# Performance work log

Measured on AMD Instinct MI355X. Metric: run time of the kernel, lower is better.

The kernel has to match this reference:

```python
import jax, jax.numpy as jnp
import numpy as np
from math import sqrt

NUM_HEADS = 16
NUM_KV_HEADS = 4
ROPE_BASE = 10000.0


def setup_inputs() -> dict:
    key = jax.random.key(0)
    ks = jax.random.split(key, 9)
    B, S, E = 4, 2048, 2048
    KV_DIM = NUM_KV_HEADS * (E // NUM_HEADS)  # 512
    s = 0.02
    return {
        "x": jax.random.normal(ks[0], (B, S, E), jnp.float32),
        "wq": jax.random.normal(ks[1], (E, E), jnp.float32) * s,
        "bq": jnp.zeros((E,), jnp.float32),
        "wk": jax.random.normal(ks[2], (KV_DIM, E), jnp.float32) * s,
        "bk": jnp.zeros((KV_DIM,), jnp.float32),
        "wv": jax.random.normal(ks[3], (KV_DIM, E), jnp.float32) * s,
        "bv": jnp.zeros((KV_DIM,), jnp.float32),
        "wo": jax.random.normal(ks[4], (E, E), jnp.float32) * s,
        "bo": jnp.zeros((E,), jnp.float32),
    }


def _rope_cos_sin(seq_len, head_dim, dtype):
    inv_freq = 1.0 / (ROPE_BASE ** (jnp.arange(0, head_dim, 2, dtype=jnp.float32) / head_dim))
    pos = jnp.arange(seq_len, dtype=jnp.float32)
    freqs = pos[:, None] * inv_freq[None, :]            # [S, D/2]
    emb = jnp.concatenate([freqs, freqs], axis=-1)      # [S, D]
    return jnp.cos(emb).astype(dtype), jnp.sin(emb).astype(dtype)


def _apply_rope(t, cos, sin):
    # t: [B, H, S, D]; cos/sin: [S, D]
    d2 = t.shape[-1] // 2
    rot = jnp.concatenate([-t[..., d2:], t[..., :d2]], axis=-1)
    return t * cos[None, None, :, :] + rot * sin[None, None, :, :]


def reference(x, wq, bq, wk, bk, wv, bv, wo, bo):
    B, S, E = x.shape
    H, KV = NUM_HEADS, NUM_KV_HEADS
    D = E // H
    G = H // KV

    q = (x @ wq.T + bq).reshape(B, S, H, D).transpose(0, 2, 1, 3)   # [B,H,S,D]
    k = (x @ wk.T + bk).reshape(B, S, KV, D).transpose(0, 2, 1, 3)  # [B,KV,S,D]
    v = (x @ wv.T + bv).reshape(B, S, KV, D).transpose(0, 2, 1, 3)

    cos, sin = _rope_cos_sin(S, D, x.dtype)
    q = _apply_rope(q, cos, sin)
    k = _apply_rope(k, cos, sin)

    # GQA: expand each kv head group_size times (contiguous repeat)
    k = jnp.repeat(k, G, axis=1)  # [B,H,S,D]
    v = jnp.repeat(v, G, axis=1)

    scores = jnp.einsum("bhqd,bhkd->bhqk", q, k)
    causal = jnp.triu(jnp.ones((S, S), dtype=bool), k=1)
    scores = jnp.where(causal[None, None, :, :], -jnp.inf, scores)
    attn = jax.nn.softmax(scores / sqrt(D), axis=-1)
    out = jnp.einsum("bhqk,bhkd->bhqd", attn, v)        # [B,H,S,D]
    out = out.transpose(0, 2, 1, 3).reshape(B, S, E)
    return out @ wo.T + bo
```

## Files before the change

kernel.cpp:

```cpp
#include <hip/hip_runtime.h>
#include <stdint.h>
#include <math.h>

typedef __attribute__((ext_vector_type(8))) short s16x8;
typedef __attribute__((ext_vector_type(4))) short s16x4;
typedef __attribute__((ext_vector_type(4))) float f32x4;
typedef __attribute__((ext_vector_type(16))) float f32x16;

#define NEGH (-1.0e30f)

__device__ __forceinline__ short f2bf(float f) {
  union { float f; unsigned int i; } c; c.f = f;
  unsigned int lsb = (c.i >> 16) & 1u;
  c.i += 0x7fffu + lsb;
  return (short)(c.i >> 16);
}
__device__ __forceinline__ float bf2f(short u) {
  union { unsigned int i; float f; } c;
  c.i = ((unsigned int)(unsigned short)u) << 16;
  return c.f;
}

#define GLOAD_LDS16(gp, lp)                                                  \
  __builtin_amdgcn_global_load_lds(                                          \
      (__attribute__((address_space(1))) void*)(void*)(gp),                  \
      (__attribute__((address_space(3))) void*)(lp), 16, 0, 0)

__global__ __launch_bounds__(256) void cvt_kernel(const float* __restrict__ in,
                                                  short* __restrict__ out)
{
  const size_t i = ((size_t)blockIdx.x * 256 + threadIdx.x) * 4;
  const float4 v = *(const float4*)(in + i);
  s16x4 o = { f2bf(v.x), f2bf(v.y), f2bf(v.z), f2bf(v.w) };
  *(s16x4*)(out + i) = o;
}

__global__ __launch_bounds__(256) void wcvt_kernel(
    const float* __restrict__ wq, const float* __restrict__ wk,
    const float* __restrict__ wv, short* __restrict__ wqb,
    short* __restrict__ wkb, short* __restrict__ wvb,
    float2* __restrict__ tab)
{
  const int bid = blockIdx.x;
  if (bid < 6144) {
    const float* in; short* out; int lb;
    if (bid < 4096)      { in = wq; out = wqb; lb = bid; }
    else if (bid < 5120) { in = wk; out = wkb; lb = bid - 4096; }
    else                 { in = wv; out = wvb; lb = bid - 5120; }
    const size_t i = ((size_t)lb * 256 + threadIdx.x) * 4;
    const float4 v = *(const float4*)(in + i);
    s16x4 o = { f2bf(v.x), f2bf(v.y), f2bf(v.z), f2bf(v.w) };
    *(s16x4*)(out + i) = o;
  } else {
    const int i = (bid - 6144) * 256 + threadIdx.x;
    const int d = i & 63;
    const float fr = (float)(i >> 6) * exp2f((float)d * -0.20762050593048584f);
    float sn, cs;
    sincosf(fr, &sn, &cs);
    tab[i] = make_float2(cs, sn);
  }
}

__global__ __launch_bounds__(256) void gemm_bt(
    const short* __restrict__ A, const short* __restrict__ W,
    const float* __restrict__ bias, const float* __restrict__ bias2,
    void* __restrict__ C, void* __restrict__ C2,
    int M, int N, int K, int omode)
{
  __shared__ __align__(16) short As[128 * 64];
  __shared__ __align__(16) short Bs[128 * 64];

  const int t = threadIdx.x;
  const int l = t & 63;
  const int w = t >> 6;
  const int lane16 = l & 15;
  const int quad = l >> 4;
  const int wm = w >> 1, wn = w & 1;

  int bx = blockIdx.x, by = blockIdx.y;
  if (gridDim.x == 8 && gridDim.y == 64) {
    const int lid = blockIdx.x + 8 * blockIdx.y;
    const int xcd = lid & 7, idx = lid >> 3;
    by = xcd * 8 + (idx >> 3);
    bx = idx & 7;
  }
  const int mb0 = by * 128;
  const int nb0 = bx * 128;

  const f32x4 zero = {0.f, 0.f, 0.f, 0.f};
  f32x4 acc[4][4];
#pragma unroll
  for (int i = 0; i < 4; ++i)
#pragma unroll
    for (int j = 0; j < 4; ++j) acc[i][j] = zero;

  const int sr = t >> 3;
  const int sp = t & 7;
  const short* Ag = A + (size_t)(mb0 + sr) * K + sp * 8;
  const short* Wg = W + (size_t)(nb0 + sr) * K + sp * 8;
  short* Al = As + t * 8;
  short* Bl = Bs + t * 8;

  const int nkt = K >> 6;
  for (int kt = 0; kt < nkt; ++kt) {
    __syncthreads();
    const int kof = kt * 64;
#pragma unroll
    for (int it = 0; it < 4; ++it) {
      GLOAD_LDS16(Ag + kof + (size_t)(it * 32) * K, Al + it * 2048);
      GLOAD_LDS16(Wg + kof + (size_t)(it * 32) * K, Bl + it * 2048);
    }
    __syncthreads();
#pragma unroll
    for (int kk = 0; kk < 2; ++kk) {
      s16x8 af[4], bf[4];
#pragma unroll
      for (int mi = 0; mi < 4; ++mi)
        af[mi] = *(const s16x8*)&As[(wm * 64 + mi * 16 + lane16) * 64 +
                                    kk * 32 + quad * 8];
#pragma unroll
      for (int ni = 0; ni < 4; ++ni)
        bf[ni] = *(const s16x8*)&Bs[(wn * 64 + ni * 16 + lane16) * 64 +
                                    kk * 32 + quad * 8];
#pragma unroll
      for (int mi = 0; mi < 4; ++mi)
#pragma unroll
        for (int ni = 0; ni < 4; ++ni)
          acc[mi][ni] = __builtin_amdgcn_mfma_f32_16x16x32_bf16(
              af[mi], bf[ni], acc[mi][ni], 0, 0, 0);
    }
  }

#pragma unroll
  for (int ni = 0; ni < 4; ++ni) {
    const int n = nb0 + wn * 64 + ni * 16 + lane16;
    const float bvx = (omode == 3 && n >= 512) ? bias2[n - 512] : bias[n];
#pragma unroll
    for (int mi = 0; mi < 4; ++mi) {
      const int m0 = mb0 + wm * 64 + mi * 16 + quad * 4;
#pragma unroll
      for (int r = 0; r < 4; ++r) {
        const int m = m0 + r;
        const float v = acc[mi][ni][r] + bvx;
        if (omode == 0) {
          ((short*)C)[(size_t)m * N + n] = f2bf(v);
        } else if (omode == 1) {
          ((float*)C)[(size_t)m * N + n] = v;
        } else {
          if (n < 512) ((short*)C)[(size_t)m * 512 + n] = f2bf(v);
          else         ((short*)C2)[(size_t)m * 512 + (n - 512)] = f2bf(v);
        }
      }
    }
  }
}

__global__ __launch_bounds__(512, 2) void gemm256_bt(
    const short* __restrict__ A, const short* __restrict__ W,
    const float* __restrict__ bias, void* __restrict__ C,
    int M, int N, int K, int omode)
{
  __shared__ __align__(16) short Asm[2 * 16384];
  __shared__ __align__(16) short Bsm[2 * 16384];

  const int t = threadIdx.x;
  const int l = t & 63;
  const int w = t >> 6;
  const int lane16 = l & 15;
  const int quad = l >> 4;
  const int wm = w >> 2;
  const int wn = w & 3;

  int bx = blockIdx.x, by = blockIdx.y;
  if (gridDim.x == 8 && gridDim.y == 32) {
    const int bid = blockIdx.y * 8 + blockIdx.x;
    const int xcd = bid & 7, idx = bid >> 3;
    const int xc = xcd & 3, yc = xcd >> 2;
    bx = xc * 2 + (idx & 1);
    by = yc * 16 + (idx >> 1);
  }
  const int mb0 = by * 256;
  const int nb0 = bx * 256;

  const f32x4 zero = {0.f, 0.f, 0.f, 0.f};
  f32x4 acc[8][4];
#pragma unroll
  for (int i = 0; i < 8; ++i)
#pragma unroll
    for (int j = 0; j < 4; ++j) acc[i][j] = zero;

  const int srow = t >> 2;
  const int scs = (t & 3) ^ ((t >> 3) & 3);
  const short* Ag = A + (size_t)(mb0 + srow) * K + scs * 8;
  const short* Wg = W + (size_t)(nb0 + srow) * K + scs * 8;
  const size_t rstep = (size_t)128 * K;

#define STAGE_A(b, kt, kh)                                                    \
  do {                                                                        \
    const size_t ko_ = (size_t)(kt) * 64 + (kh) * 32;                         \
    GLOAD_LDS16(Ag + ko_,         Asm + (b) * 16384 + (kh) * 8192 + t * 8);   \
    GLOAD_LDS16(Ag + ko_ + rstep, Asm + (b) * 16384 + (kh) * 8192 + 4096 + t * 8); \
  } while (0)
#define STAGE_B(b, kt, kh)                                                    \
  do {                                                                        \
    const size_t ko_ = (size_t)(kt) * 64 + (kh) * 32;                         \
    GLOAD_LDS16(Wg + ko_,         Bsm + (b) * 16384 + (kh) * 8192 + t * 8);   \
    GLOAD_LDS16(Wg + ko_ + rstep, Bsm + (b) * 16384 + (kh) * 8192 + 4096 + t * 8); \
  } while (0)

#define VMW6                                                                  \
  asm volatile("s_waitcnt vmcnt(6)" ::: "memory");                            \
  __builtin_amdgcn_sched_barrier(0);

  s16x8 bfr[4];

#define DO_PHASE(BUF, KK, MG, READB, STAGE_STMT, VM_STMT)                     \
  {                                                                           \
    const short* Abase = Asm + (BUF) * 16384 + (KK) * 8192;                   \
    const short* Bbase = Bsm + (BUF) * 16384 + (KK) * 8192;                   \
    if (READB) {                                                              \
      _Pragma("unroll")                                                       \
      for (int ni = 0; ni < 4; ++ni) {                                        \
        const int nr = wn * 64 + ni * 16 + lane16;                            \
        bfr[ni] = *(const s16x8*)(Bbase + nr * 32 +                           \
                                  ((quad ^ ((nr >> 1) & 3)) << 3));           \
      }                                                                       \
    }                                                                         \
    s16x8 afr[4];                                                             \
    _Pragma("unroll")                                                         \
    for (int mi2 = 0; mi2 < 4; ++mi2) {                                       \
      const int mr = wm * 128 + (MG) * 64 + mi2 * 16 + lane16;                \
      afr[mi2] = *(const s16x8*)(Abase + mr * 32 +                            \
                                 ((quad ^ ((mr >> 1) & 3)) << 3));            \
    }                                                                         \
    STAGE_STMT;                                                               \
    __builtin_amdgcn_s_barrier();                                             \
    asm volatile("s_waitcnt lgkmcnt(0)" ::: "memory");                        \
    __builtin_amdgcn_sched_barrier(0);                                        \
    __builtin_amdgcn_s_setprio(1);                                            \
    _Pragma("unroll")                                                         \
    for (int mi2 = 0; mi2 < 4; ++mi2)                                         \
      _Pragma("unroll")                                                       \
      for (int ni = 0; ni < 4; ++ni)                                          \
        acc[(MG) * 4 + mi2][ni] = __builtin_amdgcn_mfma_f32_16x16x32_bf16(    \
            afr[mi2], bfr[ni], acc[(MG) * 4 + mi2][ni], 0, 0, 0);             \
    __builtin_amdgcn_s_setprio(0);                                            \
    VM_STMT                                                                   \
    __builtin_amdgcn_s_barrier();                                             \
  }

  const int NT = K >> 6;

  STAGE_B(0, 0, 0); STAGE_A(0, 0, 0); STAGE_B(0, 0, 1); STAGE_A(0, 0, 1);
  STAGE_B(1, 1, 0); STAGE_A(1, 1, 0); STAGE_B(1, 1, 1);
  asm volatile("s_waitcnt vmcnt(6)" ::: "memory");
  __builtin_amdgcn_sched_barrier(0);
  __builtin_amdgcn_s_barrier();

  for (int i2 = 0; i2 < NT; i2 += 2) {
    const int tp1 = (i2 + 1 < NT) ? i2 + 1 : NT - 1;
    const int tp2 = (i2 + 2 < NT) ? i2 + 2 : NT - 1;
    const int tp3 = (i2 + 3 < NT) ? i2 + 3 : NT - 1;
    DO_PHASE(0, 0, 0, true,  STAGE_A(1, tp1, 1), )
    DO_PHASE(0, 0, 1, false, STAGE_B(0, tp2, 0), )
    DO_PHASE(0, 1, 0, true,  STAGE_A(0, tp2, 0), )
    DO_PHASE(0, 1, 1, false, STAGE_B(0, tp2, 1), VMW6)
    DO_PHASE(1, 0, 0, true,  STAGE_A(0, tp2, 1), )
    DO_PHASE(1, 0, 1, false, STAGE_B(1, tp3, 0), )
    DO_PHASE(1, 1, 0, true,  STAGE_A(1, tp3, 0), )
    DO_PHASE(1, 1, 1, false, STAGE_B(1, tp3, 1), VMW6)
  }

#pragma unroll
  for (int ni = 0; ni < 4; ++ni) {
    const int n = nb0 + wn * 64 + ni * 16 + lane16;
    const float bv = bias[n];
#pragma unroll
    for (int mi = 0; mi < 8; ++mi) {
      const int m0 = mb0 + wm * 128 + mi * 16 + quad * 4;
#pragma unroll
      for (int r = 0; r < 4; ++r) {
        const float v = acc[mi][ni][r] + bv;
        if (omode == 0) ((short*)C)[(size_t)(m0 + r) * N + n] = f2bf(v);
        else            ((float*)C)[(size_t)(m0 + r) * N + n] = v;
      }
    }
  }
#undef DO_PHASE
#undef STAGE_A
#undef STAGE_B
#undef VMW6
}

__global__ __launch_bounds__(256) void rope_kernel(short* __restrict__ buf,
                                                   int lognh,
                                                   const float2* __restrict__ tab)
{
  const int idx = blockIdx.x * 256 + threadIdx.x;
  const int d = idx & 63;
  const int rest = idx >> 6;
  const int row = rest >> lognh;
  const int pos = row & 2047;
  const float2 cssn = tab[(pos << 6) | d];
  const float cs = cssn.x, sn = cssn.y;
  const size_t base = (size_t)rest * 128 + d;
  const float lo = bf2f(buf[base]);
  const float hi = bf2f(buf[base + 64]);
  buf[base]      = f2bf(lo * cs - hi * sn);
  buf[base + 64] = f2bf(hi * cs + lo * sn);
}

__global__ __launch_bounds__(256) void trans_kernel(const short* __restrict__ in,
                                                    short* __restrict__ out)
{
  __shared__ short T[64 * 72];
  const int t = threadIdx.x;
  const int ms = blockIdx.x * 64;
  const int ns = blockIdx.y * 64;
  const int b = ms >> 11;
  const int sl = ms & 2047;
  const int r = t >> 3, sg = t & 7;
#pragma unroll
  for (int j = 0; j < 2; ++j) {
    const uint4 v = *(const uint4*)(in + (size_t)(ms + r + 32 * j) * 512 + ns + sg * 8);
    *(uint4*)&T[(r + 32 * j) * 72 + sg * 8] = v;
  }
  __syncthreads();
#pragma unroll
  for (int j = 0; j < 2; ++j) {
    const int nr = r + 32 * j;
    s16x8 v;
#pragma unroll
    for (int i = 0; i < 8; ++i) v[i] = T[(sg * 8 + i) * 72 + nr];
    *(s16x8*)(out + ((size_t)(b * 512 + ns + nr)) * 2048 + sl + sg * 8) = v;
  }
}

__global__ __launch_bounds__(256, 2) void attn_kernel(
    const short* __restrict__ qg, const short* __restrict__ kg,
    const short* __restrict__ vtg, short* __restrict__ og,
    const float2* __restrict__ tab)
{
  __shared__ __align__(16) short Ksm[2 * 64 * 128];
  __shared__ __align__(16) short Vsm[2 * 128 * 64];

  const int t = threadIdx.x;
  const int l = t & 63;
  const int w = t >> 6;
  const int l31 = l & 31;
  const int h2 = l >> 5;

  const int lid = blockIdx.x + 8 * (blockIdx.y + 16 * blockIdx.z);
  const int xcd = lid & 7, idx = lid >> 3;
  const int g = xcd * 2 + (idx >> 5);
  const int wv_ = idx & 31;
  const int b = g >> 2, kv = g & 3;
  const int h = kv * 4 + (wv_ >> 3);
  const int jb = wv_ & 7;

  const int krow0 = t >> 4, kseg = (t & 15) ^ (t >> 4);
  const int vrow0 = t >> 3, vseg = (t & 7) ^ ((t >> 3) & 7);

  const short* kbaseptr = kg + ((size_t)(b * 2048)) * 512 + kv * 128;
  const short* vbaseptr = vtg + ((size_t)(b * 512 + kv * 128)) * 2048;

  const float SC = 0.08838834764831845f * 1.4426950408889634f;
  const f32x16 zero16 = {0.f,0.f,0.f,0.f,0.f,0.f,0.f,0.f,
                         0.f,0.f,0.f,0.f,0.f,0.f,0.f,0.f};

#define STAGET(c)                                                             \
  do {                                                                        \
    GLOAD_LDS16(ksrc,          Ksm + (c) * 8192 + t * 8);                     \
    GLOAD_LDS16(ksrc + 8192,   Ksm + (c) * 8192 + 2048 + t * 8);              \
    GLOAD_LDS16(ksrc + 16384,  Ksm + (c) * 8192 + 4096 + t * 8);              \
    GLOAD_LDS16(ksrc + 24576,  Ksm + (c) * 8192 + 6144 + t * 8);              \
    GLOAD_LDS16(vsrc,          Vsm + (c) * 8192 + t * 8);                     \
    GLOAD_LDS16(vsrc + 65536,  Vsm + (c) * 8192 + 2048 + t * 8);              \
    GLOAD_LDS16(vsrc + 131072, Vsm + (c) * 8192 + 4096 + t * 8);              \
    GLOAD_LDS16(vsrc + 196608, Vsm + (c) * 8192 + 6144 + t * 8);              \
    ksrc += 64 * 512;                                                         \
    vsrc += 64;                                                               \
  } while (0)

  for (int sp2 = 0; sp2 < 2; ++sp2) {
    const int jj = sp2 ? (15 - jb) : jb;
    const int qb0 = jj * 128;
    const int qw0 = qb0 + w * 32;
    const int qmaxw = qw0 + 31;
    const int ntl = 2 * jj + 2;

    const short* ksrc = kbaseptr + (size_t)krow0 * 512 + kseg * 8;
    const short* vsrc = vbaseptr + (size_t)vrow0 * 2048 + vseg * 8;

    s16x8 qf[8];
    {
      const int pos = qw0 + l31;
      const short* qrow =
          qg + ((size_t)(b * 2048 + pos)) * 2048 + h * 128 + 8 * h2;
      s16x8 qr[8];
#pragma unroll
      for (int m = 0; m < 8; ++m) qr[m] = *(const s16x8*)(qrow + 16 * m);
      const float2* tb = tab + (((size_t)pos) << 6) + 8 * h2;
#pragma unroll
      for (int m = 0; m < 4; ++m) {
        float lo[8], hi[8];
#pragma unroll
        for (int j = 0; j < 8; ++j) {
          const float2 cs2 = tb[16 * m + j];
          const float l0 = bf2f(qr[m][j]);
          const float h0 = bf2f(qr[m + 4][j]);
          lo[j] = l0 * cs2.x - h0 * cs2.y;
          hi[j] = h0 * cs2.x + l0 * cs2.y;
        }
        union { unsigned int u[4]; s16x8 v; } plo, phi;
#pragma unroll
        for (int j = 0; j < 4; ++j) {
          asm("v_cvt_pk_bf16_f32 %0, %1, %2"
              : "=v"(plo.u[j]) : "v"(lo[2 * j]), "v"(lo[2 * j + 1]));
          asm("v_cvt_pk_bf16_f32 %0, %1, %2"
              : "=v"(phi.u[j]) : "v"(hi[2 * j]), "v"(hi[2 * j + 1]));
        }
        qf[m] = plo.v;
        qf[m + 4] = phi.v;
      }
    }

    f32x16 o32[4];
#pragma unroll
    for (int nb = 0; nb < 4; ++nb) o32[nb] = zero16;
    float m_i = NEGH, l_i = 0.f;

    STAGET(0);
    __syncthreads();
    int cur = 0;

    for (int tl = 0; tl < ntl; ++tl) {
      const int kbase = tl * 64;
      if (tl + 1 < ntl) STAGET(cur ^ 1);

      if (kbase <= qmaxw) {
        const short* Kb = Ksm + cur * 8192;
        const short* Vb = Vsm + cur * 8192;

        f32x16 st0 = zero16, st1 = zero16;
        __builtin_amdgcn_s_setprio(1);
#pragma unroll
        for (int m = 0; m < 8; ++m) {
          const int ch = ((2 * m + h2) ^ (l & 15)) * 8;
          const s16x8 a0 = *(const s16x8*)&Kb[l31 * 128 + ch];
          const s16x8 a1 = *(const s16x8*)&Kb[(32 + l31) * 128 + ch];
          st0 = __builtin_amdgcn_mfma_f32_32x32x16_bf16(a0, qf[m], st0, 0, 0, 0);
          st1 = __builtin_amdgcn_mfma_f32_32x32x16_bf16(a1, qf[m], st1, 0, 0, 0);
        }
        __builtin_amdgcn_s_setprio(0);

        const bool maskt = (kbase + 63 > qw0);
        const int qabs = qw0 + l31;
        if (maskt) {
#pragma unroll
          for (int r = 0; r < 16; ++r) {
            const int krow = (r & 3) + 8 * (r >> 2) + 4 * h2;
            if (kbase + krow > qabs) st0[r] = NEGH;
            if (kbase + 32 + krow > qabs) st1[r] = NEGH;
          }
        }
        float tm = NEGH;
#pragma unroll
        for (int r = 0; r < 16; ++r) tm = fmaxf(tm, fmaxf(st0[r], st1[r]));
        float tl_ = fmaxf(tm, __shfl_xor(tm, 32));
        const float mnew = fmaxf(m_i, tl_);
        if (!__all(tl_ <= m_i)) {
          const float alpha = exp2f((m_i - mnew) * SC);
          l_i *= alpha;
#pragma unroll
          for (int r = 0; r < 16; ++r) {
            const int qrow = (r & 3) + 8 * (r >> 2) + 4 * h2;
            const float ar = __shfl(alpha, qrow);
#pragma unroll
            for (int nb = 0; nb < 4; ++nb) o32[nb][r] *= ar;
          }
        }
        m_i = mnew;
        const float mS = mnew * SC;
        float rs = 0.f;
#pragma unroll
        for (int r = 0; r < 16; ++r) {
          st0[r] = exp2f(fmaf(st0[r], SC, -mS));
          st1[r] = exp2f(fmaf(st1[r], SC, -mS));
          rs += st0[r] + st1[r];
        }
        rs += __shfl_xor(rs, 32);
        l_i += rs;

        unsigned int wA[8], wB[8];
#pragma unroll
        for (int a = 0; a < 4; ++a) {
          asm("v_cvt_pk_bf16_f32 %0, %1, %2"
              : "=v"(wA[a]) : "v"(st0[4 * a]), "v"(st0[4 * a + 1]));
          asm("v_cvt_pk_bf16_f32 %0, %1, %2"
              : "=v"(wB[a]) : "v"(st0[4 * a + 2]), "v"(st0[4 * a + 3]));
          asm("v_cvt_pk_bf16_f32 %0, %1, %2"
              : "=v"(wA[a + 4]) : "v"(st1[4 * a]), "v"(st1[4 * a + 1]));
          asm("v_cvt_pk_bf16_f32 %0, %1, %2"
              : "=v"(wB[a + 4]) : "v"(st1[4 * a + 2]), "v"(st1[4 * a + 3]));
        }

        __builtin_amdgcn_s_setprio(1);
#pragma unroll
        for (int kk = 0; kk < 4; ++kk) {
          const int i0 = 2 * (kk & 1) + 4 * (kk >> 1);
          const unsigned int sA = h2 ? wA[i0] : wA[i0 + 1];
          const unsigned int sB = h2 ? wB[i0] : wB[i0 + 1];
          const unsigned int rA = (unsigned int)__shfl_xor((int)sA, 32);
          const unsigned int rB = (unsigned int)__shfl_xor((int)sB, 32);
          union { unsigned int u[4]; s16x8 v; } pfu;
          pfu.u[0] = h2 ? rA : wA[i0];
          pfu.u[1] = h2 ? rB : wB[i0];
          pfu.u[2] = h2 ? wA[i0 + 1] : rA;
          pfu.u[3] = h2 ? wB[i0 + 1] : rB;
          const s16x8 pf = pfu.v;
#pragma unroll
          for (int nb = 0; nb < 4; ++nb) {
            const s16x8 vf = *(const s16x8*)&Vb[(nb * 32 + l31) * 64 +
                                                (((2 * kk + h2) ^ (l & 7)) * 8)];
            o32[nb] = __builtin_amdgcn_mfma_f32_32x32x16_bf16(pf, vf, o32[nb],
                                                              0, 0, 0);
          }
        }
        __builtin_amdgcn_s_setprio(0);
      }

      __syncthreads();
      cur ^= 1;
    }

#pragma unroll
    for (int r = 0; r < 16; ++r) {
      const int qrow = (r & 3) + 8 * (r >> 2) + 4 * h2;
      const float lr = __shfl(l_i, qrow);
      const float inv = 1.f / lr;
      const size_t base =
          ((size_t)(b * 2048 + qw0 + qrow)) * 2048 + h * 128 + l31;
#pragma unroll
      for (int nb = 0; nb < 4; ++nb)
        og[base + nb * 32] = f2bf(o32[nb][r] * inv);
    }
  }
#undef STAGET
}

extern "C" void kernel_launch(void* const* d_in, const int* in_sizes, int n_in,
                              void* d_out, int out_size, void* d_ws,
                              size_t ws_size, hipStream_t stream)
{
  const float* x  = (const float*)d_in[0];
  const float* wq = (const float*)d_in[1];
  const float* bq = (const float*)d_in[2];
  const float* wk = (const float*)d_in[3];
  const float* bk = (const float*)d_in[4];
  const float* wv = (const float*)d_in[5];
  const float* bv = (const float*)d_in[6];
  const float* wo = (const float*)d_in[7];
  const float* bo = (const float*)d_in[8];
  float* out = (float*)d_out;

  char* ws = (char*)d_ws;
  short* xb  = (short*)ws;
  short* wqb = (short*)(ws + (32ull << 20));
  short* wkb = (short*)(ws + (40ull << 20));
  short* wvb = (short*)(ws + (42ull << 20));
  short* qws = (short*)(ws + (44ull << 20));
  float2* tab = (float2*)(ws + (76ull << 20));
  short* wob = xb;
  short* kws = (short*)d_out;
  short* vtw = (short*)((char*)d_out + (8ull << 20));
  short* vtmp = (short*)((char*)d_out + (16ull << 20));

  const dim3 blk(256);
  cvt_kernel<<<16384, blk, 0, stream>>>(x, xb);
  wcvt_kernel<<<6656, blk, 0, stream>>>(wq, wk, wv, wqb, wkb, wvb, tab);
  gemm256_bt<<<dim3(8, 32), dim3(512), 0, stream>>>(xb, wqb, bq, qws, 8192, 2048, 2048, 0);
  gemm_bt<<<dim3(8, 64), blk, 0, stream>>>(xb, wkb, bk, bv, kws, vtmp, 8192, 1024, 2048, 3);
  trans_kernel<<<dim3(128, 8), blk, 0, stream>>>(vtmp, vtw);
  rope_kernel<<<8192, blk, 0, stream>>>(kws, 2, tab);
  cvt_kernel<<<4096, blk, 0, stream>>>(wo, wob);
  attn_kernel<<<dim3(8, 16, 4), blk, 0, stream>>>(qws, kws, vtw, qws, tab);
  gemm256_bt<<<dim3(8, 32), dim3(512), 0, stream>>>(qws, wob, bo, out, 8192, 2048, 2048, 1);
}
```

Before: 495.1 us.

## Single-buffer attention K/V tiles with split K/V staging, one query block per CTA

```diff
diff --git a/kernel.cpp b/kernel.cpp
--- a/kernel.cpp
+++ b/kernel.cpp
@@ -341,8 +341,8 @@
     const short* __restrict__ vtg, short* __restrict__ og,
     const float2* __restrict__ tab)
 {
-  __shared__ __align__(16) short Ksm[2 * 64 * 128];
-  __shared__ __align__(16) short Vsm[2 * 128 * 64];
+  __shared__ __align__(16) short Ksm[64 * 128];
+  __shared__ __align__(16) short Vsm[128 * 64];
 
   const int t = threadIdx.x;
   const int l = t & 63;
@@ -350,13 +350,13 @@
   const int l31 = l & 31;
   const int h2 = l >> 5;
 
-  const int lid = blockIdx.x + 8 * (blockIdx.y + 16 * blockIdx.z);
+  const int lid = blockIdx.x + 16 * (blockIdx.y + 16 * blockIdx.z);
   const int xcd = lid & 7, idx = lid >> 3;
-  const int g = xcd * 2 + (idx >> 5);
-  const int wv_ = idx & 31;
+  const int g = xcd * 2 + (idx >> 6);
+  const int wv_ = idx & 63;
   const int b = g >> 2, kv = g & 3;
-  const int h = kv * 4 + (wv_ >> 3);
-  const int jb = wv_ & 7;
+  const int h = kv * 4 + (wv_ >> 4);
+  const int jj = wv_ & 15;
 
   const int krow0 = t >> 4, kseg = (t & 15) ^ (t >> 4);
   const int vrow0 = t >> 3, vseg = (t & 7) ^ ((t >> 3) & 7);
@@ -368,185 +368,188 @@
   const f32x16 zero16 = {0.f,0.f,0.f,0.f,0.f,0.f,0.f,0.f,
                          0.f,0.f,0.f,0.f,0.f,0.f,0.f,0.f};
 
-#define STAGET(c)                                                             \
+#define STAGE_K()                                                             \
   do {                                                                        \
-    GLOAD_LDS16(ksrc,          Ksm + (c) * 8192 + t * 8);                     \
-    GLOAD_LDS16(ksrc + 8192,   Ksm + (c) * 8192 + 2048 + t * 8);              \
-    GLOAD_LDS16(ksrc + 16384,  Ksm + (c) * 8192 + 4096 + t * 8);              \
-    GLOAD_LDS16(ksrc + 24576,  Ksm + (c) * 8192 + 6144 + t * 8);              \
-    GLOAD_LDS16(vsrc,          Vsm + (c) * 8192 + t * 8);                     \
-    GLOAD_LDS16(vsrc + 65536,  Vsm + (c) * 8192 + 2048 + t * 8);              \
-    GLOAD_LDS16(vsrc + 131072, Vsm + (c) * 8192 + 4096 + t * 8);              \
-    GLOAD_LDS16(vsrc + 196608, Vsm + (c) * 8192 + 6144 + t * 8);              \
+    GLOAD_LDS16(ksrc,          Ksm + t * 8);                                  \
+    GLOAD_LDS16(ksrc + 8192,   Ksm + 2048 + t * 8);                           \
+    GLOAD_LDS16(ksrc + 16384,  Ksm + 4096 + t * 8);                           \
+    GLOAD_LDS16(ksrc + 24576,  Ksm + 6144 + t * 8);                           \
     ksrc += 64 * 512;                                                         \
+  } while (0)
+#define STAGE_V()                                                             \
+  do {                                                                        \
+    GLOAD_LDS16(vsrc,          Vsm + t * 8);                                  \
+    GLOAD_LDS16(vsrc + 65536,  Vsm + 2048 + t * 8);                           \
+    GLOAD_LDS16(vsrc + 131072, Vsm + 4096 + t * 8);                           \
+    GLOAD_LDS16(vsrc + 196608, Vsm + 6144 + t * 8);                           \
     vsrc += 64;                                                               \
   } while (0)
 
-  for (int sp2 = 0; sp2 < 2; ++sp2) {
-    const int jj = sp2 ? (15 - jb) : jb;
-    const int qb0 = jj * 128;
-    const int qw0 = qb0 + w * 32;
-    const int qmaxw = qw0 + 31;
-    const int ntl = 2 * jj + 2;
-
-    const short* ksrc = kbaseptr + (size_t)krow0 * 512 + kseg * 8;
-    const short* vsrc = vbaseptr + (size_t)vrow0 * 2048 + vseg * 8;
-
-    s16x8 qf[8];
-    {
-      const int pos = qw0 + l31;
-      const short* qrow =
-          qg + ((size_t)(b * 2048 + pos)) * 2048 + h * 128 + 8 * h2;
-      s16x8 qr[8];
-#pragma unroll
-      for (int m = 0; m < 8; ++m) qr[m] = *(const s16x8*)(qrow + 16 * m);
-      const float2* tb = tab + (((size_t)pos) << 6) + 8 * h2;
-#pragma unroll
-      for (int m = 0; m < 4; ++m) {
-        float lo[8], hi[8];
-#pragma unroll
-        for (int j = 0; j < 8; ++j) {
-          const float2 cs2 = tb[16 * m + j];
-          const float l0 = bf2f(qr[m][j]);
-          const float h0 = bf2f(qr[m + 4][j]);
-          lo[j] = l0 * cs2.x - h0 * cs2.y;
-          hi[j] = h0 * cs2.x + l0 * cs2.y;
+  const int qb0 = jj * 128;
+  const int qw0 = qb0 + w * 32;
+  const int qmaxw = qw0 + 31;
+  const int ntl = 2 * jj + 2;
+
+  const short* ksrc = kbaseptr + (size_t)krow0 * 512 + kseg * 8;
+  const short* vsrc = vbaseptr + (size_t)vrow0 * 2048 + vseg * 8;
+
+  s16x8 qf[8];
+  {
+    const int pos = qw0 + l31;
+    const short* qrow =
+        qg + ((size_t)(b * 2048 + pos)) * 2048 + h * 128 + 8 * h2;
+    s16x8 qr[8];
+#pragma unroll
+    for (int m = 0; m < 8; ++m) qr[m] = *(const s16x8*)(qrow + 16 * m);
+    const float2* tb = tab + (((size_t)pos) << 6) + 8 * h2;
+#pragma unroll
+    for (int m = 0; m < 4; ++m) {
+      float lo[8], hi[8];
+#pragma unroll
+      for (int j = 0; j < 8; ++j) {
+        const float2 cs2 = tb[16 * m + j];
+        const float l0 = bf2f(qr[m][j]);
+        const float h0 = bf2f(qr[m + 4][j]);
+        lo[j] = l0 * cs2.x - h0 * cs2.y;
+        hi[j] = h0 * cs2.x + l0 * cs2.y;
+      }
+      union { unsigned int u[4]; s16x8 v; } plo, phi;
+#pragma unroll
+      for (int j = 0; j < 4; ++j) {
+        asm("v_cvt_pk_bf16_f32 %0, %1, %2"
+            : "=v"(plo.u[j]) : "v"(lo[2 * j]), "v"(lo[2 * j + 1]));
+        asm("v_cvt_pk_bf16_f32 %0, %1, %2"
+            : "=v"(phi.u[j]) : "v"(hi[2 * j]), "v"(hi[2 * j + 1]));
+      }
+      qf[m] = plo.v;
+      qf[m + 4] = phi.v;
+    }
+  }
+
+  f32x16 o32[4];
+#pragma unroll
+  for (int nb = 0; nb < 4; ++nb) o32[nb] = zero16;
+  float m_i = NEGH, l_i = 0.f;
+
+  STAGE_K();
+  STAGE_V();
+  __syncthreads();
+
+  for (int tl = 0; tl < ntl; ++tl) {
+    const int kbase = tl * 64;
+    const bool cmp = (kbase <= qmaxw);
+
+    f32x16 st0 = zero16, st1 = zero16;
+    if (cmp) {
+      __builtin_amdgcn_s_setprio(1);
+#pragma unroll
+      for (int m = 0; m < 8; ++m) {
+        const int ch = ((2 * m + h2) ^ (l & 15)) * 8;
+        const s16x8 a0 = *(const s16x8*)&Ksm[l31 * 128 + ch];
+        const s16x8 a1 = *(const s16x8*)&Ksm[(32 + l31) * 128 + ch];
+        st0 = __builtin_amdgcn_mfma_f32_32x32x16_bf16(a0, qf[m], st0, 0, 0, 0);
+        st1 = __builtin_amdgcn_mfma_f32_32x32x16_bf16(a1, qf[m], st1, 0, 0, 0);
+      }
+      __builtin_amdgcn_s_setprio(0);
+    }
+
+    __syncthreads();
+    if (tl + 1 < ntl) STAGE_K();
+
+    if (cmp) {
+      const bool maskt = (kbase + 63 > qw0);
+      const int qabs = qw0 + l31;
+      if (maskt) {
+#pragma unroll
+        for (int r = 0; r < 16; ++r) {
+          const int krow = (r & 3) + 8 * (r >> 2) + 4 * h2;
+          if (kbase + krow > qabs) st0[r] = NEGH;
+          if (kbase + 32 + krow > qabs) st1[r] = NEGH;
         }
-        union { unsigned int u[4]; s16x8 v; } plo, phi;
-#pragma unroll
-        for (int j = 0; j < 4; ++j) {
-          asm("v_cvt_pk_bf16_f32 %0, %1, %2"
-              : "=v"(plo.u[j]) : "v"(lo[2 * j]), "v"(lo[2 * j + 1]));
-          asm("v_cvt_pk_bf16_f32 %0, %1, %2"
-              : "=v"(phi.u[j]) : "v"(hi[2 * j]), "v"(hi[2 * j + 1]));
+      }
+      float tm = NEGH;
+#pragma unroll
+      for (int r = 0; r < 16; ++r) tm = fmaxf(tm, fmaxf(st0[r], st1[r]));
+      float tl_ = fmaxf(tm, __shfl_xor(tm, 32));
+      const float mnew = fmaxf(m_i, tl_);
+      if (!__all(tl_ <= m_i)) {
+        const float alpha = exp2f((m_i - mnew) * SC);
+        l_i *= alpha;
+#pragma unroll
+        for (int r = 0; r < 16; ++r) {
+          const int qrow = (r & 3) + 8 * (r >> 2) + 4 * h2;
+          const float ar = __shfl(alpha, qrow);
+#pragma unroll
+          for (int nb = 0; nb < 4; ++nb) o32[nb][r] *= ar;
         }
-        qf[m] = plo.v;
-        qf[m + 4] = phi.v;
-      }
-    }
-
-    f32x16 o32[4];
-#pragma unroll
-    for (int nb = 0; nb < 4; ++nb) o32[nb] = zero16;
-    float m_i = NEGH, l_i = 0.f;
-
-    STAGET(0);
+      }
+      m_i = mnew;
+      const float mS = mnew * SC;
+      float rs = 0.f;
+#pragma unroll
+      for (int r = 0; r < 16; ++r) {
+        st0[r] = exp2f(fmaf(st0[r], SC, -mS));
+        st1[r] = exp2f(fmaf(st1[r], SC, -mS));
+        rs += st0[r] + st1[r];
+      }
+      rs += __shfl_xor(rs, 32);
+      l_i += rs;
+
+      unsigned int wA[8], wB[8];
+#pragma unroll
+      for (int a = 0; a < 4; ++a) {
+        asm("v_cvt_pk_bf16_f32 %0, %1, %2"
+            : "=v"(wA[a]) : "v"(st0[4 * a]), "v"(st0[4 * a + 1]));
+        asm("v_cvt_pk_bf16_f32 %0, %1, %2"
+            : "=v"(wB[a]) : "v"(st0[4 * a + 2]), "v"(st0[4 * a + 3]));
+        asm("v_cvt_pk_bf16_f32 %0, %1, %2"
+            : "=v"(wA[a + 4]) : "v"(st1[4 * a]), "v"(st1[4 * a + 1]));
+        asm("v_cvt_pk_bf16_f32 %0, %1, %2"
+            : "=v"(wB[a + 4]) : "v"(st1[4 * a + 2]), "v"(st1[4 * a + 3]));
+      }
+
+      __builtin_amdgcn_s_setprio(1);
+#pragma unroll
+      for (int kk = 0; kk < 4; ++kk) {
+        const int i0 = 2 * (kk & 1) + 4 * (kk >> 1);
+        const unsigned int sA = h2 ? wA[i0] : wA[i0 + 1];
+        const unsigned int sB = h2 ? wB[i0] : wB[i0 + 1];
+        const unsigned int rA = (unsigned int)__shfl_xor((int)sA, 32);
+        const unsigned int rB = (unsigned int)__shfl_xor((int)sB, 32);
+        union { unsigned int u[4]; s16x8 v; } pfu;
+        pfu.u[0] = h2 ? rA : wA[i0];
+        pfu.u[1] = h2 ? rB : wB[i0];
+        pfu.u[2] = h2 ? wA[i0 + 1] : rA;
+        pfu.u[3] = h2 ? wB[i0 + 1] : rB;
+        const s16x8 pf = pfu.v;
+#pragma unroll
+        for (int nb = 0; nb < 4; ++nb) {
+          const s16x8 vf = *(const s16x8*)&Vsm[(nb * 32 + l31) * 64 +
+                                               (((2 * kk + h2) ^ (l & 7)) * 8)];
+          o32[nb] = __builtin_amdgcn_mfma_f32_32x32x16_bf16(pf, vf, o32[nb],
+                                                            0, 0, 0);
+        }
+      }
+      __builtin_amdgcn_s_setprio(0);
+    }
+
     __syncthreads();
-    int cur = 0;
-
-    for (int tl = 0; tl < ntl; ++tl) {
-      const int kbase = tl * 64;
-      if (tl + 1 < ntl) STAGET(cur ^ 1);
-
-      if (kbase <= qmaxw) {
-        const short* Kb = Ksm + cur * 8192;
-        const short* Vb = Vsm + cur * 8192;
-
-        f32x16 st0 = zero16, st1 = zero16;
-        __builtin_amdgcn_s_setprio(1);
-#pragma unroll
-        for (int m = 0; m < 8; ++m) {
-          const int ch = ((2 * m + h2) ^ (l & 15)) * 8;
-          const s16x8 a0 = *(const s16x8*)&Kb[l31 * 128 + ch];
-          const s16x8 a1 = *(const s16x8*)&Kb[(32 + l31) * 128 + ch];
-          st0 = __builtin_amdgcn_mfma_f32_32x32x16_bf16(a0, qf[m], st0, 0, 0, 0);
-          st1 = __builtin_amdgcn_mfma_f32_32x32x16_bf16(a1, qf[m], st1, 0, 0, 0);
-        }
-        __builtin_amdgcn_s_setprio(0);
-
-        const bool maskt = (kbase + 63 > qw0);
-        const int qabs = qw0 + l31;
-        if (maskt) {
-#pragma unroll
-          for (int r = 0; r < 16; ++r) {
-            const int krow = (r & 3) + 8 * (r >> 2) + 4 * h2;
-            if (kbase + krow > qabs) st0[r] = NEGH;
-            if (kbase + 32 + krow > qabs) st1[r] = NEGH;
-          }
-        }
-        float tm = NEGH;
-#pragma unroll
-        for (int r = 0; r < 16; ++r) tm = fmaxf(tm, fmaxf(st0[r], st1[r]));
-        float tl_ = fmaxf(tm, __shfl_xor(tm, 32));
-        const float mnew = fmaxf(m_i, tl_);
-        if (!__all(tl_ <= m_i)) {
-          const float alpha = exp2f((m_i - mnew) * SC);
-          l_i *= alpha;
-#pragma unroll
-          for (int r = 0; r < 16; ++r) {
-            const int qrow = (r & 3) + 8 * (r >> 2) + 4 * h2;
-            const float ar = __shfl(alpha, qrow);
-#pragma unroll
-            for (int nb = 0; nb < 4; ++nb) o32[nb][r] *= ar;
-          }
-        }
-        m_i = mnew;
-        const float mS = mnew * SC;
-        float rs = 0.f;
-#pragma unroll
-        for (int r = 0; r < 16; ++r) {
-          st0[r] = exp2f(fmaf(st0[r], SC, -mS));
-          st1[r] = exp2f(fmaf(st1[r], SC, -mS));
-          rs += st0[r] + st1[r];
-        }
-        rs += __shfl_xor(rs, 32);
-        l_i += rs;
-
-        unsigned int wA[8], wB[8];
-#pragma unroll
-        for (int a = 0; a < 4; ++a) {
-          asm("v_cvt_pk_bf16_f32 %0, %1, %2"
-              : "=v"(wA[a]) : "v"(st0[4 * a]), "v"(st0[4 * a + 1]));
-          asm("v_cvt_pk_bf16_f32 %0, %1, %2"
-              : "=v"(wB[a]) : "v"(st0[4 * a + 2]), "v"(st0[4 * a + 3]));
-          asm("v_cvt_pk_bf16_f32 %0, %1, %2"
-              : "=v"(wA[a + 4]) : "v"(st1[4 * a]), "v"(st1[4 * a + 1]));
-          asm("v_cvt_pk_bf16_f32 %0, %1, %2"
-              : "=v"(wB[a + 4]) : "v"(st1[4 * a + 2]), "v"(st1[4 * a + 3]));
-        }
-
-        __builtin_amdgcn_s_setprio(1);
-#pragma unroll
-        for (int kk = 0; kk < 4; ++kk) {
-          const int i0 = 2 * (kk & 1) + 4 * (kk >> 1);
-          const unsigned int sA = h2 ? wA[i0] : wA[i0 + 1];
-          const unsigned int sB = h2 ? wB[i0] : wB[i0 + 1];
-          const unsigned int rA = (unsigned int)__shfl_xor((int)sA, 32);
-          const unsigned int rB = (unsigned int)__shfl_xor((int)sB, 32);
-          union { unsigned int u[4]; s16x8 v; } pfu;
-          pfu.u[0] = h2 ? rA : wA[i0];
-          pfu.u[1] = h2 ? rB : wB[i0];
-          pfu.u[2] = h2 ? wA[i0 + 1] : rA;
-          pfu.u[3] = h2 ? wB[i0 + 1] : rB;
-          const s16x8 pf = pfu.v;
-#pragma unroll
-          for (int nb = 0; nb < 4; ++nb) {
-            const s16x8 vf = *(const s16x8*)&Vb[(nb * 32 + l31) * 64 +
-                                                (((2 * kk + h2) ^ (l & 7)) * 8)];
-            o32[nb] = __builtin_amdgcn_mfma_f32_32x32x16_bf16(pf, vf, o32[nb],
-                                                              0, 0, 0);
-          }
-        }
-        __builtin_amdgcn_s_setprio(0);
-      }
-
-      __syncthreads();
-      cur ^= 1;
-    }
-
-#pragma unroll
-    for (int r = 0; r < 16; ++r) {
-      const int qrow = (r & 3) + 8 * (r >> 2) + 4 * h2;
-      const float lr = __shfl(l_i, qrow);
-      const float inv = 1.f / lr;
-      const size_t base =
-          ((size_t)(b * 2048 + qw0 + qrow)) * 2048 + h * 128 + l31;
-#pragma unroll
-      for (int nb = 0; nb < 4; ++nb)
-        og[base + nb * 32] = f2bf(o32[nb][r] * inv);
-    }
-  }
-#undef STAGET
+    if (tl + 1 < ntl) STAGE_V();
+  }
+
+#pragma unroll
+  for (int r = 0; r < 16; ++r) {
+    const int qrow = (r & 3) + 8 * (r >> 2) + 4 * h2;
+    const float lr = __shfl(l_i, qrow);
+    const float inv = 1.f / lr;
+    const size_t base =
+        ((size_t)(b * 2048 + qw0 + qrow)) * 2048 + h * 128 + l31;
+#pragma unroll
+    for (int nb = 0; nb < 4; ++nb)
+      og[base + nb * 32] = f2bf(o32[nb][r] * inv);
+  }
+#undef STAGE_K
+#undef STAGE_V
 }
 
 extern "C" void kernel_launch(void* const* d_in, const int* in_sizes, int n_in,
@@ -584,6 +587,6 @@
   trans_kernel<<<dim3(128, 8), blk, 0, stream>>>(vtmp, vtw);
   rope_kernel<<<8192, blk, 0, stream>>>(kws, 2, tab);
   cvt_kernel<<<4096, blk, 0, stream>>>(wo, wob);
-  attn_kernel<<<dim3(8, 16, 4), blk, 0, stream>>>(qws, kws, vtw, qws, tab);
+  attn_kernel<<<dim3(16, 16, 4), blk, 0, stream>>>(qws, kws, vtw, qws, tab);
   gemm256_bt<<<dim3(8, 32), dim3(512), 0, stream>>>(qws, wob, bo, out, 8192, 2048, 2048, 1);
 }
```

New measurement: 544.3 us. 1.1x slower.
